# Kernel tuning notes

Measured on AMD Instinct MI355X. Metric: run time of the kernel, lower is better.

## Reference

```python
import jax, jax.numpy as jnp
import numpy as np

# static multi-scale feature pyramid (strides 8/16/32/64 of ~800px input)
SPATIAL = ((100, 100), (50, 50), (25, 25), (13, 13))
L = 4          # num_levels
NH = 8         # num_heads
NP = 4         # num_points
E = 256        # embed_dim
HD = E // NH   # head dim = 32
NLAYERS = 6
FFN_DIM = 1024
T = sum(h * w for h, w in SPATIAL)  # 13294 total tokens
B = 2


def _layer_norm(x, g, b, eps=1e-5):
    m = jnp.mean(x, -1, keepdims=True)
    v = jnp.mean((x - m) ** 2, -1, keepdims=True)
    return (x - m) * jax.lax.rsqrt(v + eps) * g + b


def _get_reference_points(valid_ratios):
    # valid_ratios: [B, L, 2] (wx, hy)
    refs = []
    for lvl, (H_, W_) in enumerate(SPATIAL):
        ry, rx = jnp.meshgrid(
            jnp.linspace(0.5, H_ - 0.5, H_, dtype=jnp.float32),
            jnp.linspace(0.5, W_ - 0.5, W_, dtype=jnp.float32),
            indexing='ij')
        ry = ry.reshape(-1)[None] / (valid_ratios[:, None, lvl, 1] * H_)
        rx = rx.reshape(-1)[None] / (valid_ratios[:, None, lvl, 0] * W_)
        refs.append(jnp.stack([rx, ry], -1))            # [B, H*W, 2]
    ref = jnp.concatenate(refs, 1)                       # [B, T, 2]
    return ref[:, :, None] * valid_ratios[:, None]       # [B, T, L, 2]


def _msda(value, loc, attn_w):
    # value: [B, T, NH, HD]; loc: [B, Q, NH, L, NP, 2] in [0,1]; attn_w: [B, Q, NH, L, NP]
    Bv, Tv, H, D = value.shape
    Q = loc.shape[1]
    out = jnp.zeros((Bv, Q, H, D), value.dtype)
    start = 0
    for lvl, (h, w) in enumerate(SPATIAL):
        v = value[:, start:start + h * w].transpose(0, 2, 1, 3)  # [B, NH, hw, D]
        start += h * w
        g = loc[:, :, :, lvl]                                    # [B, Q, NH, NP, 2]
        # grid_sample semantics, align_corners=False: pixel = g*size - 0.5
        x = g[..., 0] * w - 0.5
        y = g[..., 1] * h - 0.5
        x0 = jnp.floor(x).astype(jnp.int32)
        y0 = jnp.floor(y).astype(jnp.int32)
        wx = x - x0
        wy = y - y0

        def corner(ix, iy, cw):
            valid = (ix >= 0) & (ix < w) & (iy >= 0) & (iy < h)
            idx = jnp.clip(iy, 0, h - 1) * w + jnp.clip(ix, 0, w - 1)  # [B,Q,NH,NP]
            idx_t = idx.transpose(0, 2, 1, 3).reshape(Bv, H, Q * NP)
            gath = jnp.take_along_axis(v, idx_t[..., None], axis=2)    # [B,NH,QP,D]
            gath = gath.reshape(Bv, H, Q, NP, D)
            m = valid.transpose(0, 2, 1, 3)[..., None].astype(value.dtype)
            cw_t = cw.transpose(0, 2, 1, 3)[..., None]
            return gath * m * cw_t

        samp = (corner(x0, y0, (1 - wx) * (1 - wy))
                + corner(x0 + 1, y0, wx * (1 - wy))
                + corner(x0, y0 + 1, (1 - wx) * wy)
                + corner(x0 + 1, y0 + 1, wx * wy))  # [B,NH,Q,NP,D]
        out = out + jnp.einsum('bhqpd,bqhp->bqhd', samp, attn_w[:, :, :, lvl])
    return out.reshape(Bv, Q, H * D)


# offset normalizer (W, H) per level, as in Deformable-DETR
_OFF_NORM = jnp.array([[w, h] for (h, w) in SPATIAL], jnp.float32)  # [L, 2]


def _block(src, pos, ref, mask, p):
    (Wv, bv, Woff, boff, Wattn, battn, Wout, bout,
     n1g, n1b, n2g, n2b, W1, b1, W2, b2) = p
    x = _layer_norm(src, n1g, n1b)
    q = x + pos
    value = x @ Wv + bv
    value = jnp.where(mask[:, :, None], 0.0, value).reshape(B, T, NH, HD)
    off = (q @ Woff + boff).reshape(B, T, NH, L, NP, 2)
    attn = (q @ Wattn + battn).reshape(B, T, NH, L * NP)
    attn = jax.nn.softmax(attn, -1).reshape(B, T, NH, L, NP)
    loc = ref[:, :, None, :, None, :] + off / _OFF_NORM[None, None, None, :, None, :]
    attn_out = _msda(value, loc, attn) @ Wout + bout
    src = src + attn_out
    x = _layer_norm(src, n2g, n2b)
    ffn = jax.nn.relu(x @ W1 + b1) @ W2 + b2
    return src + ffn


def setup_inputs() -> dict:
    key = jax.random.key(0)
    ks = jax.random.split(key, 24)

    def rn(k, shape, scale=0.02):
        return jax.random.normal(k, shape, jnp.float32) * scale

    inp = {
        'src': jax.random.normal(ks[0], (B, T, E), jnp.float32),
        'pos': jax.random.normal(ks[1], (B, T, E), jnp.float32),
        'valid_ratios': jnp.ones((B, L, 2), jnp.float32),
        'spatial_shapes': jnp.array(SPATIAL, jnp.int32),
        'level_start_index': jnp.array(
            np.concatenate([[0], np.cumsum([h * w for h, w in SPATIAL])[:-1]]), jnp.int32),
        'mask': jnp.zeros((B, T), bool),
        # per-layer stacked parameters [NLAYERS, ...]
        'Wv': rn(ks[2], (NLAYERS, E, E)),
        'bv': jnp.zeros((NLAYERS, E), jnp.float32),
        'Woff': rn(ks[3], (NLAYERS, E, NH * L * NP * 2)),
        'boff': rn(ks[4], (NLAYERS, NH * L * NP * 2), 0.5),
        'Wattn': rn(ks[5], (NLAYERS, E, NH * L * NP)),
        'battn': jnp.zeros((NLAYERS, NH * L * NP), jnp.float32),
        'Wout': rn(ks[6], (NLAYERS, E, E)),
        'bout': jnp.zeros((NLAYERS, E), jnp.float32),
        'n1g': jnp.ones((NLAYERS, E), jnp.float32),
        'n1b': jnp.zeros((NLAYERS, E), jnp.float32),
        'n2g': jnp.ones((NLAYERS, E), jnp.float32),
        'n2b': jnp.zeros((NLAYERS, E), jnp.float32),
        'W1': rn(ks[7], (NLAYERS, E, FFN_DIM)),
        'b1': jnp.zeros((NLAYERS, FFN_DIM), jnp.float32),
        'W2': rn(ks[8], (NLAYERS, FFN_DIM, E)),
        'b2': jnp.zeros((NLAYERS, E), jnp.float32),
    }
    return inp


def reference(src, pos, valid_ratios, spatial_shapes, level_start_index, mask,
              Wv, bv, Woff, boff, Wattn, battn, Wout, bout,
              n1g, n1b, n2g, n2b, W1, b1, W2, b2):
    # spatial_shapes / level_start_index are encoded statically in SPATIAL (values match)
    ref = _get_reference_points(valid_ratios)  # [B, T, L, 2]
    x = src
    stacked = (Wv, bv, Woff, boff, Wattn, battn, Wout, bout,
               n1g, n1b, n2g, n2b, W1, b1, W2, b2)
    for i in range(NLAYERS):
        p = tuple(a[i] for a in stacked)
        x = _block(x, pos, ref, mask, p)
    return x
```

## Files before the change

### kernel.cpp

```cpp
#include <hip/hip_runtime.h>
#include <hip/hip_bf16.h>

#define NLAYERS 6
#define Bc 2
#define Tc 13294
#define Ec 256
#define NHc 8
#define FFNc 1024

#define EPI_BIAS 0
#define EPI_MASK 1
#define EPI_RES  2
#define EPI_RELU 3
#define EPI_VALOA 4

typedef __attribute__((ext_vector_type(8))) short bf16x8;
typedef __attribute__((ext_vector_type(4))) float f32x4;

typedef __attribute__((address_space(3))) unsigned int u32_lds;
typedef __attribute__((address_space(1))) unsigned int u32_glb;

__device__ __forceinline__ void gld16(const void* g, void* l) {
    __builtin_amdgcn_global_load_lds((const u32_glb*)g, (u32_lds*)l, 16, 0, 0);
}

__device__ __forceinline__ short f2bf(float f) {
    union { float f; unsigned u; } v; v.f = f;
    unsigned r = v.u + 0x7FFFu + ((v.u >> 16) & 1u);
    return (short)(r >> 16);
}
__device__ __forceinline__ float bf2f(short s) {
    union { unsigned u; float f; } v; v.u = ((unsigned)(unsigned short)s) << 16;
    return v.f;
}
__device__ __forceinline__ float bf_lo(unsigned u) {
    union { unsigned u; float f; } v; v.u = u << 16; return v.f;
}

__global__ __launch_bounds__(256) void ln_kernel(
    const float* __restrict__ src, const float* __restrict__ pos,
    const float* __restrict__ g, const float* __restrict__ b,
    short* __restrict__ x, short* __restrict__ q, int rows)
{
    int wave = threadIdx.x >> 6;
    int lane = threadIdx.x & 63;
    int row = blockIdx.x * 4 + wave;
    if (row >= rows) return;
    const float* p = src + (size_t)row * Ec;
    float4 v = *(const float4*)(p + lane * 4);
    float s  = v.x + v.y + v.z + v.w;
    float sq = v.x*v.x + v.y*v.y + v.z*v.z + v.w*v.w;
    #pragma unroll
    for (int o = 32; o; o >>= 1) { s += __shfl_xor(s, o); sq += __shfl_xor(sq, o); }
    float mean = s * (1.f / Ec);
    float var  = sq * (1.f / Ec) - mean * mean;
    float inv  = rsqrtf(var + 1e-5f);
    float4 gg = *(const float4*)(g + lane * 4);
    float4 bb = *(const float4*)(b + lane * 4);
    float xo0 = (v.x - mean) * inv * gg.x + bb.x;
    float xo1 = (v.y - mean) * inv * gg.y + bb.y;
    float xo2 = (v.z - mean) * inv * gg.z + bb.z;
    float xo3 = (v.w - mean) * inv * gg.w + bb.w;
    short4 xs; xs.x = f2bf(xo0); xs.y = f2bf(xo1); xs.z = f2bf(xo2); xs.w = f2bf(xo3);
    *(short4*)(x + (size_t)row * Ec + lane * 4) = xs;
    float4 pp = *(const float4*)(pos + (size_t)row * Ec + lane * 4);
    short4 qs;
    qs.x = f2bf(xo0 + pp.x); qs.y = f2bf(xo1 + pp.y);
    qs.z = f2bf(xo2 + pp.z); qs.w = f2bf(xo3 + pp.w);
    *(short4*)(q + (size_t)row * Ec + lane * 4) = qs;
}

__global__ __launch_bounds__(256) void ln_bf_kernel(
    const short* __restrict__ src, const float* __restrict__ pos,
    const float* __restrict__ g, const float* __restrict__ b,
    short* __restrict__ x, short* __restrict__ q, int rows)
{
    int wave = threadIdx.x >> 6;
    int lane = threadIdx.x & 63;
    int row = blockIdx.x * 4 + wave;
    if (row >= rows) return;
    short4 v4 = *(const short4*)(src + (size_t)row * Ec + lane * 4);
    float v0 = bf2f(v4.x), v1 = bf2f(v4.y), v2 = bf2f(v4.z), v3 = bf2f(v4.w);
    float s  = v0 + v1 + v2 + v3;
    float sq = v0*v0 + v1*v1 + v2*v2 + v3*v3;
    #pragma unroll
    for (int o = 32; o; o >>= 1) { s += __shfl_xor(s, o); sq += __shfl_xor(sq, o); }
    float mean = s * (1.f / Ec);
    float var  = sq * (1.f / Ec) - mean * mean;
    float inv  = rsqrtf(var + 1e-5f);
    float4 gg = *(const float4*)(g + lane * 4);
    float4 bb = *(const float4*)(b + lane * 4);
    float xo0 = (v0 - mean) * inv * gg.x + bb.x;
    float xo1 = (v1 - mean) * inv * gg.y + bb.y;
    float xo2 = (v2 - mean) * inv * gg.z + bb.z;
    float xo3 = (v3 - mean) * inv * gg.w + bb.w;
    short4 xs; xs.x = f2bf(xo0); xs.y = f2bf(xo1); xs.z = f2bf(xo2); xs.w = f2bf(xo3);
    *(short4*)(x + (size_t)row * Ec + lane * 4) = xs;
    if (q) {
        float4 pp = *(const float4*)(pos + (size_t)row * Ec + lane * 4);
        short4 qs;
        qs.x = f2bf(xo0 + pp.x); qs.y = f2bf(xo1 + pp.y);
        qs.z = f2bf(xo2 + pp.z); qs.w = f2bf(xo3 + pp.w);
        *(short4*)(q + (size_t)row * Ec + lane * 4) = qs;
    }
}

__global__ __launch_bounds__(256) void transpose_all(
    const float* __restrict__ Wv,   const float* __restrict__ Woff,
    const float* __restrict__ Wattn,const float* __restrict__ Wout,
    const float* __restrict__ W1,   const float* __restrict__ W2,
    short* __restrict__ wcT, short* __restrict__ woutT,
    short* __restrict__ w1T, short* __restrict__ w2T)
{
    __shared__ float tile[32][33];
    const int l = blockIdx.z;
    const int t = blockIdx.x;
    const float* W; short* Wt; int K, N, lstr, rowOff, n0, k0;
    if (t < 64)       { W = Wv;    Wt = wcT;   K = 256;  N = 256;  lstr = 163840; rowOff = 0;
                        int u = t;        n0 = (u & 7) * 32;  k0 = (u >> 3) * 32; }
    else if (t < 128) { W = Woff;  Wt = wcT;   K = 256;  N = 256;  lstr = 163840; rowOff = 256;
                        int u = t - 64;   n0 = (u & 7) * 32;  k0 = (u >> 3) * 32; }
    else if (t < 160) { W = Wattn; Wt = wcT;   K = 256;  N = 128;  lstr = 163840; rowOff = 512;
                        int u = t - 128;  n0 = (u & 3) * 32;  k0 = (u >> 2) * 32; }
    else if (t < 224) { W = Wout;  Wt = woutT; K = 256;  N = 256;  lstr = 65536;  rowOff = 0;
                        int u = t - 160;  n0 = (u & 7) * 32;  k0 = (u >> 3) * 32; }
    else if (t < 480) { W = W1;    Wt = w1T;   K = 256;  N = 1024; lstr = 262144; rowOff = 0;
                        int u = t - 224;  n0 = (u & 31) * 32; k0 = (u >> 5) * 32; }
    else              { W = W2;    Wt = w2T;   K = 1024; N = 256;  lstr = 262144; rowOff = 0;
                        int u = t - 480;  n0 = (u & 7) * 32;  k0 = (u >> 3) * 32; }
    const float* Wl = W + (size_t)l * K * N;
    short* Wtl = Wt + (size_t)l * lstr;
    int tx = threadIdx.x & 31, ty = threadIdx.x >> 5;
    #pragma unroll
    for (int i = 0; i < 32; i += 8)
        tile[ty + i][tx] = Wl[(size_t)(k0 + ty + i) * N + n0 + tx];
    __syncthreads();
    #pragma unroll
    for (int i = 0; i < 32; i += 8)
        Wtl[(size_t)(rowOff + n0 + ty + i) * K + k0 + tx] = f2bf(tile[tx][ty + i]);
}

template<int EPI, int OBF, int RESBF>
__global__ __launch_bounds__(256) void gemm_mfma(
    const short* __restrict__ A, const short* __restrict__ A2,
    const short* __restrict__ Bt,
    const float* __restrict__ bias, const float* __restrict__ bias2,
    const float* __restrict__ bias3,
    const float* __restrict__ resf, const short* __restrict__ resb,
    const unsigned char* __restrict__ mask,
    void* __restrict__ Cout, void* __restrict__ Cout2, int M, int N, int K)
{
    __shared__ short As[2][128 * 32];
    __shared__ short Bs[2][64 * 32];
    const int tid = threadIdx.x;
    const int lane = tid & 63;
    const int wv = tid >> 6;
    const int row0 = blockIdx.x * 128;
    const int col0 = blockIdx.y * 64;
    const int mbase = (wv >> 1) * 64;
    const int nbase = (wv & 1) * 32;
    const int lr = lane & 15;
    const int kg = lane >> 4;

    const short* Ause = (EPI == EPI_VALOA && blockIdx.y >= 4) ? A2 : A;

    f32x4 zf = {0.f, 0.f, 0.f, 0.f};
    f32x4 acc[4][2];
    #pragma unroll
    for (int i = 0; i < 4; ++i)
        #pragma unroll
        for (int j = 0; j < 2; ++j) acc[i][j] = zf;

    const int scol = (lane & 3) * 8;
    const int srowA = wv * 32 + (lane >> 2);
    const short* Ap = Ause + (size_t)(row0 + srowA) * K + scol;
    const int lA0 = srowA * 32 + scol;
    const int lA1 = lA0 + 16 * 32;
    const int srowB = wv * 16 + (lane >> 2);
    const short* Bp = Bt + (size_t)(col0 + srowB) * K + scol;
    const int lB = srowB * 32 + scol;

    #define STAGE(buf, k0) do { \
        gld16(Ap + (k0),                &As[buf][lA0]); \
        gld16(Ap + (size_t)16*K + (k0), &As[buf][lA1]); \
        gld16(Bp + (k0),                &Bs[buf][lB]); \
    } while (0)

    STAGE(0, 0);
    __syncthreads();
    int cur = 0;
    for (int k0 = 0; k0 < K; k0 += 32) {
        if (k0 + 32 < K) STAGE(cur ^ 1, k0 + 32);
        bf16x8 af[4], bfr[2];
        #pragma unroll
        for (int i = 0; i < 4; ++i)
            af[i]  = *(const bf16x8*)&As[cur][(mbase + i * 16 + lr) * 32 + kg * 8];
        #pragma unroll
        for (int j = 0; j < 2; ++j)
            bfr[j] = *(const bf16x8*)&Bs[cur][(nbase + j * 16 + lr) * 32 + kg * 8];
        #pragma unroll
        for (int mi = 0; mi < 4; ++mi)
            #pragma unroll
            for (int ni = 0; ni < 2; ++ni)
                acc[mi][ni] = __builtin_amdgcn_mfma_f32_16x16x32_bf16(
                    af[mi], bfr[ni], acc[mi][ni], 0, 0, 0);
        __syncthreads();
        cur ^= 1;
    }
    #undef STAGE

    float* Cf = (float*)Cout;
    short* Cb = (short*)Cout;
    short* Vb = (short*)Cout2;
    #pragma unroll
    for (int ni = 0; ni < 2; ++ni) {
        int col = col0 + nbase + ni * 16 + lr;
        float bz;
        if (EPI == EPI_VALOA)
            bz = (col < 256) ? bias[col] : ((col < 512) ? bias2[col - 256] : bias3[col - 512]);
        else
            bz = (bias2 && col >= 256) ? bias2[col - 256] : bias[col];
        #pragma unroll
        for (int mi = 0; mi < 4; ++mi) {
            int rb = row0 + mbase + mi * 16 + kg * 4;
            #pragma unroll
            for (int j = 0; j < 4; ++j) {
                int grow = rb + j;
                if (grow >= M) continue;
                float v = acc[mi][ni][j] + bz;
                if (EPI == EPI_VALOA) {
                    if (col < 256) {
                        if (mask[grow]) v = 0.f;
                        Vb[(size_t)grow * 256 + col] = f2bf(v);
                    } else {
                        Cb[(size_t)grow * 384 + (col - 256)] = f2bf(v);
                    }
                    continue;
                }
                if (EPI == EPI_MASK) { if (mask[grow]) v = 0.f; }
                if (EPI == EPI_RES) {
                    v += RESBF ? bf2f(resb[(size_t)grow * N + col])
                               : resf[(size_t)grow * N + col];
                }
                if (EPI == EPI_RELU) v = v > 0.f ? v : 0.f;
                if (OBF) Cb[(size_t)grow * N + col] = f2bf(v);
                else     Cf[(size_t)grow * N + col] = v;
            }
        }
    }
}

__global__ __launch_bounds__(256) void msda_kernel(
    const short* __restrict__ value, const short* __restrict__ oa,
    const float* __restrict__ vr, short* __restrict__ out)
{
    __shared__ int pts[8 * 136];
    const int t = threadIdx.x;
    const int bq = blockIdx.x;
    const int b = (bq >= Tc) ? 1 : 0;
    const int qq = bq - b * Tc;

    if (t < 128) {
        const int g = t >> 4;
        const int p = t & 15;
        const int lvl = p >> 2;
        const int St[4] = {0, 10000, 12500, 13125};
        int qi, Wq, qlvl;
        if (qq < 10000)      { qlvl = 0; qi = qq;         Wq = 100; }
        else if (qq < 12500) { qlvl = 1; qi = qq - 10000; Wq = 50; }
        else if (qq < 13125) { qlvl = 2; qi = qq - 12500; Wq = 25; }
        else                 { qlvl = 3; qi = qq - 13125; Wq = 13; }
        float base_x = (0.5f + (float)(qi % Wq)) / (vr[(b*4+qlvl)*2+0] * (float)Wq);
        float base_y = (0.5f + (float)(qi / Wq)) / (vr[(b*4+qlvl)*2+1] * (float)Wq);

        float logit = bf2f(oa[(size_t)bq * 384 + 256 + g * 16 + p]);
        float mx = logit;
        #pragma unroll
        for (int o = 8; o; o >>= 1) mx = fmaxf(mx, __shfl_xor(mx, o));
        float e = __expf(logit - mx);
        float sum = e;
        #pragma unroll
        for (int o = 8; o; o >>= 1) sum += __shfl_xor(sum, o);
        float aw = e / sum;

        const int w = (lvl == 0) ? 100 : ((lvl == 1) ? 50 : ((lvl == 2) ? 25 : 13));
        const int hh = w;
        const float wf = (float)w;
        const float refxw = base_x * vr[(b*4+lvl)*2+0] * wf;
        const float refyw = base_y * vr[(b*4+lvl)*2+1] * wf;
        const float ox = bf2f(oa[(size_t)bq * 384 + g * 32 + p * 2 + 0]);
        const float oy = bf2f(oa[(size_t)bq * 384 + g * 32 + p * 2 + 1]);
        float xf = refxw + ox - 0.5f;
        float yf = refyw + oy - 0.5f;
        float x0f = floorf(xf), y0f = floorf(yf);
        int x0 = (int)x0f, y0 = (int)y0f;
        float wx = xf - x0f, wy = yf - y0f;
        float w00 = (1.f - wx) * (1.f - wy) * aw;
        float w10 = wx * (1.f - wy) * aw;
        float w01 = (1.f - wx) * wy * aw;
        float w11 = wx * wy * aw;
        bool vx0 = (x0 >= 0) && (x0 < w);
        bool vx1 = (x0 + 1 >= 0) && (x0 + 1 < w);
        bool vy0 = (y0 >= 0) && (y0 < hh);
        bool vy1 = (y0 + 1 >= 0) && (y0 + 1 < hh);
        if (!(vx0 && vy0)) w00 = 0.f;
        if (!(vx1 && vy0)) w10 = 0.f;
        if (!(vx0 && vy1)) w01 = 0.f;
        if (!(vx1 && vy1)) w11 = 0.f;
        int cx0 = min(max(x0, 0), w - 1), cx1 = min(max(x0 + 1, 0), w - 1);
        int cy0 = min(max(y0, 0), hh - 1), cy1 = min(max(y0 + 1, 0), hh - 1);
        int rowbase = b * Tc + St[lvl];
        int slot = g * 136 + p * 8 + ((p >> 3) & 1) * 4;
        int4 wq4; wq4.x = __float_as_int(w00); wq4.y = __float_as_int(w10);
        wq4.z = __float_as_int(w01); wq4.w = __float_as_int(w11);
        int4 aq4;
        aq4.x = (rowbase + cy0 * w + cx0) * 512 + g * 64;
        aq4.y = (rowbase + cy0 * w + cx1) * 512 + g * 64;
        aq4.z = (rowbase + cy1 * w + cx0) * 512 + g * 64;
        aq4.w = (rowbase + cy1 * w + cx1) * 512 + g * 64;
        *(int4*)&pts[slot] = wq4;
        *(int4*)&pts[slot + 4] = aq4;
    }
    __syncthreads();

    const int group = t >> 5;
    const int l32 = t & 31;
    const int d4 = (l32 & 15) * 4;
    const int ph = (l32 >> 4) * 8;
    const int xw = (l32 >> 4) * 4;
    const char* vbase = (const char*)value;
    float accL = 0.f, accH = 0.f;
    #pragma unroll
    for (int j = 0; j < 8; ++j) {
        int p = ph + j;
        int slot = group * 136 + p * 8 + xw;
        int4 wq = *(const int4*)&pts[slot];
        int4 aq = *(const int4*)&pts[slot + 4];
        unsigned u0 = *(const unsigned*)(vbase + (unsigned)(aq.x + d4));
        unsigned u1 = *(const unsigned*)(vbase + (unsigned)(aq.y + d4));
        unsigned u2 = *(const unsigned*)(vbase + (unsigned)(aq.z + d4));
        unsigned u3 = *(const unsigned*)(vbase + (unsigned)(aq.w + d4));
        float w00 = __int_as_float(wq.x), w10 = __int_as_float(wq.y);
        float w01 = __int_as_float(wq.z), w11 = __int_as_float(wq.w);
        accL = fmaf(w00, bf_lo(u0), accL); accH = fmaf(w00, __int_as_float((int)u0), accH);
        accL = fmaf(w10, bf_lo(u1), accL); accH = fmaf(w10, __int_as_float((int)u1), accH);
        accL = fmaf(w01, bf_lo(u2), accL); accH = fmaf(w01, __int_as_float((int)u2), accH);
        accL = fmaf(w11, bf_lo(u3), accL); accH = fmaf(w11, __int_as_float((int)u3), accH);
    }
    accL += __shfl_xor(accL, 16);
    accH += __shfl_xor(accH, 16);
    if (l32 < 16) {
        unsigned pk = ((unsigned)(unsigned short)f2bf(accL)) |
                      (((unsigned)(unsigned short)f2bf(accH)) << 16);
        *(unsigned*)((char*)out + (size_t)bq * 512 + group * 64 + d4) = pk;
    }
}

extern "C" void kernel_launch(void* const* d_in, const int* in_sizes, int n_in,
                              void* d_out, int out_size, void* d_ws, size_t ws_size,
                              hipStream_t stream) {
    const float* src  = (const float*)d_in[0];
    const float* pos  = (const float*)d_in[1];
    const float* vr   = (const float*)d_in[2];
    const unsigned char* mask = (const unsigned char*)d_in[5];
    const float* Wv    = (const float*)d_in[6];
    const float* bv    = (const float*)d_in[7];
    const float* Woff  = (const float*)d_in[8];
    const float* boff  = (const float*)d_in[9];
    const float* Wattn = (const float*)d_in[10];
    const float* battn = (const float*)d_in[11];
    const float* Wout  = (const float*)d_in[12];
    const float* bout  = (const float*)d_in[13];
    const float* n1g   = (const float*)d_in[14];
    const float* n1b   = (const float*)d_in[15];
    const float* n2g   = (const float*)d_in[16];
    const float* n2b   = (const float*)d_in[17];
    const float* W1    = (const float*)d_in[18];
    const float* b1    = (const float*)d_in[19];
    const float* W2    = (const float*)d_in[20];
    const float* b2    = (const float*)d_in[21];
    float* out = (float*)d_out;

    const size_t R = (size_t)Bc * Tc;

    short* xb    = (short*)d_ws;
    short* qb    = xb + R * 256;
    short* valb  = qb + R * 256;
    short* msdab = valb + R * 256;
    short* oab   = msdab + R * 256;
    short* srcb  = oab + R * 384;
    short* ln2b  = xb;
    short* hb    = qb;
    short* wcT   = srcb + R * 256;
    short* woutT = wcT + 6 * 163840;
    short* w1T   = woutT + 6 * 65536;
    short* w2T   = w1T + 6 * 262144;

    transpose_all<<<dim3(736, 1, 6), 256, 0, stream>>>(
        Wv, Woff, Wattn, Wout, W1, W2, wcT, woutT, w1T, w2T);

    const int M = (int)R;
    const int lnBlocks = (int)((R + 3) / 4);
    const int MT = (int)((R + 127) / 128);

    ln_kernel<<<lnBlocks, 256, 0, stream>>>(src, pos, n1g, n1b, xb, qb, M);

    for (int l = 0; l < NLAYERS; ++l) {
        gemm_mfma<EPI_VALOA, 1, 0><<<dim3(MT, 10), 256, 0, stream>>>(
            xb, qb, wcT + (size_t)l * 163840, bv + l * Ec, boff + l * 256, battn + l * 128,
            nullptr, nullptr, mask, oab, valb, M, 640, 256);
        msda_kernel<<<(int)R, 256, 0, stream>>>(valb, oab, vr, msdab);
        if (l == 0)
            gemm_mfma<EPI_RES, 1, 0><<<dim3(MT, 4), 256, 0, stream>>>(
                msdab, nullptr, woutT + (size_t)l * 65536, bout + l * Ec, nullptr, nullptr,
                src, nullptr, nullptr, srcb, nullptr, M, 256, 256);
        else
            gemm_mfma<EPI_RES, 1, 1><<<dim3(MT, 4), 256, 0, stream>>>(
                msdab, nullptr, woutT + (size_t)l * 65536, bout + l * Ec, nullptr, nullptr,
                nullptr, srcb, nullptr, srcb, nullptr, M, 256, 256);
        ln_bf_kernel<<<lnBlocks, 256, 0, stream>>>(srcb, nullptr, n2g + l * Ec, n2b + l * Ec,
                                                   ln2b, nullptr, M);
        gemm_mfma<EPI_RELU, 1, 0><<<dim3(MT, 16), 256, 0, stream>>>(
            ln2b, nullptr, w1T + (size_t)l * 262144, b1 + l * FFNc, nullptr, nullptr,
            nullptr, nullptr, nullptr, hb, nullptr, M, 1024, 256);
        if (l < NLAYERS - 1) {
            gemm_mfma<EPI_RES, 1, 1><<<dim3(MT, 4), 256, 0, stream>>>(
                hb, nullptr, w2T + (size_t)l * 262144, b2 + l * Ec, nullptr, nullptr,
                nullptr, srcb, nullptr, srcb, nullptr, M, 256, 1024);
            ln_bf_kernel<<<lnBlocks, 256, 0, stream>>>(srcb, pos, n1g + (l + 1) * Ec,
                                                       n1b + (l + 1) * Ec, xb, qb, M);
        } else {
            gemm_mfma<EPI_RES, 0, 1><<<dim3(MT, 4), 256, 0, stream>>>(
                hb, nullptr, w2T + (size_t)l * 262144, b2 + l * Ec, nullptr, nullptr,
                nullptr, srcb, nullptr, out, nullptr, M, 256, 1024);
        }
    }
}
```

Baseline: 1.132 ms.

## Triple-buffer GEMM LDS staging with explicit vmcnt waits

Moves the MFMA GEMM from double to triple buffering in LDS. Loads are issued two k-steps ahead, and each step waits with explicit s_waitcnt vmcnt counts and raw s_barrier calls instead of a blanket __syncthreads. The aim is to keep more global-to-LDS loads in flight and hide memory latency behind the MFMAs. It raises LDS use per block, which may cut occupancy, and it relies on the hand-set vmcnt counts being correct.

Measured after the change: 1.187 ms. 1.05x slower.

```diff
diff --git a/kernel.cpp b/kernel.cpp
--- a/kernel.cpp
+++ b/kernel.cpp
@@ -150,8 +150,8 @@
     const unsigned char* __restrict__ mask,
     void* __restrict__ Cout, void* __restrict__ Cout2, int M, int N, int K)
 {
-    __shared__ short As[2][128 * 32];
-    __shared__ short Bs[2][64 * 32];
+    __shared__ short As[3][128 * 32];
+    __shared__ short Bs[3][64 * 32];
     const int tid = threadIdx.x;
     const int lane = tid & 63;
     const int wv = tid >> 6;
@@ -186,31 +186,44 @@
         gld16(Bp + (k0),                &Bs[buf][lB]); \
     } while (0)
 
+    const int nIter = K >> 5;
     STAGE(0, 0);
-    __syncthreads();
-    int cur = 0;
-    for (int k0 = 0; k0 < K; k0 += 32) {
-        if (k0 + 32 < K) STAGE(cur ^ 1, k0 + 32);
+    if (nIter > 1) STAGE(1, 32);
+
+    int cb = 0;
+    int sb = 2;
+    for (int i = 0; i < nIter; ++i) {
+        __builtin_amdgcn_s_barrier();
+        if (i + 2 < nIter) {
+            STAGE(sb, (i + 2) * 32);
+            asm volatile("s_waitcnt vmcnt(6)" ::: "memory");
+        } else if (i + 1 < nIter) {
+            asm volatile("s_waitcnt vmcnt(3)" ::: "memory");
+        } else {
+            asm volatile("s_waitcnt vmcnt(0)" ::: "memory");
+        }
+        __builtin_amdgcn_s_barrier();
+        __builtin_amdgcn_sched_barrier(0);
         bf16x8 af[4], bfr[2];
         #pragma unroll
-        for (int i = 0; i < 4; ++i)
-            af[i]  = *(const bf16x8*)&As[cur][(mbase + i * 16 + lr) * 32 + kg * 8];
-        #pragma unroll
-        for (int j = 0; j < 2; ++j)
-            bfr[j] = *(const bf16x8*)&Bs[cur][(nbase + j * 16 + lr) * 32 + kg * 8];
+        for (int ii = 0; ii < 4; ++ii)
+            af[ii]  = *(const bf16x8*)&As[cb][(mbase + ii * 16 + lr) * 32 + kg * 8];
+        #pragma unroll
+        for (int jj = 0; jj < 2; ++jj)
+            bfr[jj] = *(const bf16x8*)&Bs[cb][(nbase + jj * 16 + lr) * 32 + kg * 8];
         #pragma unroll
         for (int mi = 0; mi < 4; ++mi)
             #pragma unroll
             for (int ni = 0; ni < 2; ++ni)
                 acc[mi][ni] = __builtin_amdgcn_mfma_f32_16x16x32_bf16(
                     af[mi], bfr[ni], acc[mi][ni], 0, 0, 0);
-        __syncthreads();
-        cur ^= 1;
+        cb = (cb == 2) ? 0 : cb + 1;
+        sb = (sb == 2) ? 0 : sb + 1;
     }
     #undef STAGE
 
     float* Cf = (float*)Cout;
-    short* Cb = (short*)Cout;
+    short* Cb2 = (short*)Cout;
     short* Vb = (short*)Cout2;
     #pragma unroll
     for (int ni = 0; ni < 2; ++ni) {
@@ -233,7 +246,7 @@
                         if (mask[grow]) v = 0.f;
                         Vb[(size_t)grow * 256 + col] = f2bf(v);
                     } else {
-                        Cb[(size_t)grow * 384 + (col - 256)] = f2bf(v);
+                        Cb2[(size_t)grow * 384 + (col - 256)] = f2bf(v);
                     }
                     continue;
                 }
@@ -243,7 +256,7 @@
                                : resf[(size_t)grow * N + col];
                 }
                 if (EPI == EPI_RELU) v = v > 0.f ? v : 0.f;
-                if (OBF) Cb[(size_t)grow * N + col] = f2bf(v);
+                if (OBF) Cb2[(size_t)grow * N + col] = f2bf(v);
                 else     Cf[(size_t)grow * N + col] = v;
             }
         }
```
